# Optimization experiments

Hardware: AMD Instinct MI355X
Metric: run time of the kernel (lower is better)

## Reference

```python
import jax, jax.numpy as jnp
import numpy as np
from math import sqrt

B, L, S, H, E = 4, 2048, 2048, 8, 64
T = 1.0  # softmax temperature


def setup_inputs() -> dict:
    key = jax.random.key(0)
    kq, kk, kv = jax.random.split(key, 3)
    q = jax.random.normal(kq, (B, L, H, E), dtype=jnp.float32)
    k = jax.random.normal(kk, (B, S, H, E), dtype=jnp.float32)
    v = jax.random.normal(kv, (B, S, H, E), dtype=jnp.float32)
    mask = jnp.zeros((B, L), dtype=jnp.bool_)  # unused by the module, kept for signature fidelity
    return {"q": q, "k": k, "v": v, "mask": mask}


def reference(q, k, v, mask):
    Bq, Lq, Hq, Eq = q.shape
    # [B,L,H,E] -> [B,H,E,L]; FFT over time axis
    xq = jnp.transpose(q, (0, 2, 3, 1))
    xk = jnp.transpose(k, (0, 2, 3, 1))
    xv = jnpp_t = jnp.transpose(v, (0, 2, 3, 1))
    xq_ft = jnp.fft.rfft(xq, axis=-1, norm='ortho')   # [B,H,E,Lf]
    xk_ft = jnp.fft.rfft(xk, axis=-1, norm='ortho')   # [B,H,E,Sf]
    xv_ft = jnp.fft.rfft(xv, axis=-1, norm='ortho')   # [B,H,E,Sf]
    # complex frequency-domain scores [B,H,Lf,Sf]
    scores = jnp.einsum('bhex,bhey->bhxy', xq_ft, jnp.conj(xk_ft)) / sqrt(Eq)
    # activation == 'softmax': softmax over |scores|/T, then real-weighted complex mix
    attn = jax.nn.softmax(jnp.abs(scores) / T, axis=-1)
    xqkv_ft = jnp.einsum('bhxy,bhey->bhex', attn.astype(xv_ft.dtype), xv_ft)  # [B,H,E,Lf]
    out = jnp.fft.irfft(xqkv_ft, n=Lq, axis=-1, norm='ortho')  # [B,H,E,L]
    return jnp.transpose(out, (0, 3, 1, 2))  # [B,L,H,E]
```

## Files before the change

kernel.cpp:

```cpp
#include <hip/hip_runtime.h>
#include <hip/hip_bf16.h>
#include <math.h>

#define LOGN  11
#define NN    2048
#define LOGM  10
#define MM    1024
#define NF    1025
#define NYP   1056
#define TWO_PI 6.283185307179586f
#define INV_SQRT_N 0.022097086912079608f
#define INV_SCALE  0.044194173824159216f
#define LOG2E      1.4426950408889634f

#define PAD(i) ((i) + ((i) >> 4))
#define MMP   1088
#define TWP   816

typedef __attribute__((ext_vector_type(8))) short bhalf8;
typedef __attribute__((ext_vector_type(4))) float f32x4;

#define MFMA16(a, b, c) __builtin_amdgcn_mfma_f32_16x16x32_bf16(a, b, c, 0, 0, 0)

#define GLD16(gp, lp)                                                              \
    __builtin_amdgcn_global_load_lds(                                              \
        (const __attribute__((address_space(1))) void*)(gp),                       \
        (__attribute__((address_space(3))) void*)(lp), 16, 0, 0)

#define CVTPK(dst, lo, hi) \
    asm("v_cvt_pk_bf16_f32 %0, %1, %2" : "=v"(dst) : "v"(lo), "v"(hi))

#define EXP2F(dst, src) \
    asm("v_exp_f32 %0, %1" : "=v"(dst) : "v"(src))

__device__ __forceinline__ unsigned short f2bf(float f) {
    union { float f; unsigned u; } v; v.f = f;
    unsigned r = v.u + 0x7FFFu + ((v.u >> 16) & 1u);
    return (unsigned short)(r >> 16);
}
__device__ __forceinline__ float bf2f(unsigned short h) {
    union { unsigned u; float f; } v; v.u = ((unsigned)h) << 16;
    return v.f;
}

__device__ __forceinline__ float2 cmul(float2 x, float2 w) {
    return make_float2(x.x * w.x - x.y * w.y, x.x * w.y + x.y * w.x);
}

template<bool FWD>
__device__ __forceinline__ void r4(float2& a, float2& b, float2& c, float2& d) {
    float2 apc = make_float2(a.x + c.x, a.y + c.y);
    float2 amc = make_float2(a.x - c.x, a.y - c.y);
    float2 bpd = make_float2(b.x + d.x, b.y + d.y);
    float2 bmd = make_float2(b.x - d.x, b.y - d.y);
    a = make_float2(apc.x + bpd.x, apc.y + bpd.y);
    c = make_float2(apc.x - bpd.x, apc.y - bpd.y);
    if (FWD) {
        b = make_float2(amc.x + bmd.y, amc.y - bmd.x);
        d = make_float2(amc.x - bmd.y, amc.y + bmd.x);
    } else {
        b = make_float2(amc.x - bmd.y, amc.y + bmd.x);
        d = make_float2(amc.x + bmd.y, amc.y - bmd.x);
    }
}

template<bool FWD>
__device__ __forceinline__ void s0s1(float2 x[16], const float2* tw) {
    #pragma unroll
    for (int c = 0; c < 4; c++)
        r4<FWD>(x[c], x[4 + c], x[8 + c], x[12 + c]);
    #pragma unroll
    for (int i = 0; i < 4; i++) {
        float2 w1 = tw[PAD(64 * i)], w2 = tw[PAD(128 * i)], w3 = tw[PAD(192 * i)];
        x[4 * i + 1] = cmul(x[4 * i + 1], w1);
        x[4 * i + 2] = cmul(x[4 * i + 2], w2);
        x[4 * i + 3] = cmul(x[4 * i + 3], w3);
        r4<FWD>(x[4 * i], x[4 * i + 1], x[4 * i + 2], x[4 * i + 3]);
    }
}

template<bool FWD>
__device__ __forceinline__ void fft_mid(float2* bufS, const float2* tw, int q, int r)
{
    {
        float2 v[4][4];
        #pragma unroll
        for (int d = 0; d < 4; d++)
            #pragma unroll
            for (int c = 0; c < 4; c++)
                v[d][c] = bufS[PAD(256 * q + 64 * d + 16 * c + r)];
        float2 w1 = tw[PAD(16 * r)], w2 = tw[PAD(32 * r)], w3 = tw[PAD(48 * r)];
        #pragma unroll
        for (int d = 0; d < 4; d++) {
            v[d][1] = cmul(v[d][1], w1);
            v[d][2] = cmul(v[d][2], w2);
            v[d][3] = cmul(v[d][3], w3);
            r4<FWD>(v[d][0], v[d][1], v[d][2], v[d][3]);
        }
        #pragma unroll
        for (int c = 0; c < 4; c++) {
            int e = 4 * (16 * c + r);
            float2 u1 = tw[PAD(e)], u2 = tw[PAD(2 * e)], u3 = tw[PAD(3 * e)];
            v[1][c] = cmul(v[1][c], u1);
            v[2][c] = cmul(v[2][c], u2);
            v[3][c] = cmul(v[3][c], u3);
            r4<FWD>(v[0][c], v[1][c], v[2][c], v[3][c]);
        }
        #pragma unroll
        for (int d = 0; d < 4; d++)
            #pragma unroll
            for (int c = 0; c < 4; c++)
                bufS[PAD(256 * q + 64 * d + 16 * c + r)] = v[d][c];
    }
    __syncthreads();
    {
        #pragma unroll
        for (int k = 0; k < 4; k++) {
            int p4 = 16 * q + r + 64 * k;
            float2 a = bufS[PAD(p4)];
            float2 b = bufS[PAD(p4 + 256)];
            float2 c = bufS[PAD(p4 + 512)];
            float2 d = bufS[PAD(p4 + 768)];
            b = cmul(b, tw[PAD(p4)]);
            c = cmul(c, tw[PAD(2 * p4)]);
            d = cmul(d, tw[PAD(3 * p4)]);
            r4<FWD>(a, b, c, d);
            bufS[PAD(p4)]       = a;
            bufS[PAD(p4 + 256)] = b;
            bufS[PAD(p4 + 512)] = c;
            bufS[PAD(p4 + 768)] = d;
        }
    }
    __syncthreads();
}

__global__ __launch_bounds__(256) void tr_fwd(const float* __restrict__ q,
                                              const float* __restrict__ k,
                                              const float* __restrict__ v,
                                              unsigned short* __restrict__ ttr,
                                              float2* __restrict__ twf,
                                              float2* __restrict__ twi,
                                              float2* __restrict__ rc)
{
    __shared__ float Ts[64][65];
    int tt     = blockIdx.x;
    int h      = blockIdx.y;
    int z      = blockIdx.z;
    int tensor = z >> 2;
    int b      = z & 3;
    int tid    = threadIdx.x;
    int t0     = tt * 64;

    if (z == 0 && h == 0 && tt < 5) {
        int i = tt * 256 + tid;
        if (i < 768) {
            float ang = TWO_PI * (float)i / (float)MM;
            float sv, cv;
            __sincosf(ang, &sv, &cv);
            twf[i] = make_float2(cv, -sv);
            twi[i] = make_float2(cv,  sv);
        }
        if (i < 1025) {
            float ang = TWO_PI * (float)i / (float)NN;
            float sv, cv;
            __sincosf(ang, &sv, &cv);
            rc[i] = make_float2(cv, sv);
        }
    }

    const float* in = (tensor == 0) ? q : (tensor == 1) ? k : v;

    {
        int tl = tid >> 2, ec = (tid & 3) * 16;
        const float* src = in + ((size_t)b * 2048 + t0 + tl) * 512 + h * 64 + ec;
        #pragma unroll
        for (int m = 0; m < 4; m++) {
            float4 v4 = *(const float4*)(src + m * 4);
            Ts[tl][ec + m * 4 + 0] = v4.x;
            Ts[tl][ec + m * 4 + 1] = v4.y;
            Ts[tl][ec + m * 4 + 2] = v4.z;
            Ts[tl][ec + m * 4 + 3] = v4.w;
        }
    }
    __syncthreads();
    {
        int el = tid >> 2, tc = (tid & 3) * 16;
        size_t row = ((size_t)(tensor * 32 + b * 8 + h)) * 64 + el;
        unsigned short* dst = ttr + row * 2048 + t0 + tc;
        #pragma unroll
        for (int m = 0; m < 4; m++) {
            float a0 = Ts[tc + m * 4 + 0][el], a1 = Ts[tc + m * 4 + 1][el];
            float a2 = Ts[tc + m * 4 + 2][el], a3 = Ts[tc + m * 4 + 3][el];
            unsigned u0, u1;
            CVTPK(u0, a0, a1);
            CVTPK(u1, a2, a3);
            uint2 o; o.x = u0; o.y = u1;
            *(uint2*)(dst + m * 4) = o;
        }
    }
}

__global__ __launch_bounds__(128) void fft_fwd(const unsigned short* __restrict__ ttr,
                                               const float2* __restrict__ twg,
                                               const float2* __restrict__ rc,
                                               unsigned short* __restrict__ Pq,
                                               unsigned short* __restrict__ Pk,
                                               unsigned short* __restrict__ Pv)
{
    __shared__ float2 buf[2][MMP];
    __shared__ float2 tw[TWP];

    int g  = blockIdx.x;
    int t  = threadIdx.x;
    int w  = t >> 6, tp = t & 63;
    int q4 = tp >> 4, r = tp & 15;
    int G  = ((tp & 3) << 4) | (tp & 12) | (tp >> 4);

    int s      = 2 * g + w;
    int p      = s % 96;
    int e      = s / 96;
    int tensor = p / 32;
    int bh     = p % 32;

    unsigned short* plane = (tensor == 0) ? Pq : (tensor == 1) ? Pk : Pv;
    float scl = (tensor == 0) ? (INV_SQRT_N * 0.125f * LOG2E) : INV_SQRT_N;
    int vk3 = (tensor == 2) ? (((e >> 2) & 3) << 3) : 0;
    unsigned short* dre  = plane + ((size_t)bh * 128 + e) * NYP;
    unsigned short* dim_ = dre + (size_t)64 * NYP;
    const unsigned short* src = ttr + ((size_t)p * 64 + e) * 2048;

    #pragma unroll
    for (int i = t; i < 768; i += 128) tw[PAD(i)] = twg[i];

    float2* bufS = buf[w];

    float2 x[16];
    #pragma unroll
    for (int k = 0; k < 16; k++) {
        unsigned pr = *(const unsigned*)(src + 2 * (tp + 64 * k));
        x[k] = make_float2(bf2f((unsigned short)(pr & 0xFFFFu)),
                           bf2f((unsigned short)(pr >> 16)));
    }
    s0s1<true>(x, tw);
    #pragma unroll
    for (int k = 0; k < 16; k++)
        bufS[PAD(16 * G + 4 * (k & 3) + (k >> 2))] = x[k];
    __syncthreads();

    fft_mid<true>(bufS, tw, q4, r);

#define RPOINT(Ai, Bi, CX, CY, XR, XI) do {                                \
        float Ex = 0.5f * (Ai.x + Bi.x), Ey = 0.5f * (Ai.y - Bi.y);        \
        float Dx = 0.5f * (Ai.x - Bi.x), Dy = 0.5f * (Ai.y + Bi.y);        \
        float Ox = Dy, Oy = -Dx;                                           \
        XR = (Ex + (CX) * Ox + (CY) * Oy) * scl;                           \
        XI = (Ey + (CX) * Oy - (CY) * Ox) * scl;                           \
    } while (0)

    #pragma unroll
    for (int i = 0; i < 8; i++) {
        int kk = 2 * tp + 128 * i;
        float2 A0 = bufS[PAD(kk)];
        float2 B0 = bufS[PAD((MM - kk) & (MM - 1))];
        float2 A1 = bufS[PAD(kk + 1)];
        float2 B1 = bufS[PAD(MM - kk - 1)];
        float4 rq = *(const float4*)(&rc[kk]);
        float Xr0, Xi0, Xr1, Xi1;
        RPOINT(A0, B0, rq.x, rq.y, Xr0, Xi0);
        RPOINT(A1, B1, rq.z, rq.w, Xr1, Xi1);
        unsigned ur, ui;
        CVTPK(ur, Xr0, Xr1);
        CVTPK(ui, Xi0, Xi1);
        int ks = kk ^ vk3;
        *(unsigned*)(dre + ks)  = ur;
        *(unsigned*)(dim_ + ks) = ui;
    }
    if (tp < 16) {
        unsigned ur = 0, ui = 0;
        if (tp == 0) {
            float2 A = bufS[PAD(0)];
            float Xr = (A.x - A.y) * scl;
            float zz = 0.f;
            CVTPK(ur, Xr, zz);
        }
        int ks = (1024 + 2 * tp) ^ vk3;
        *(unsigned*)(dre + ks)  = ur;
        *(unsigned*)(dim_ + ks) = ui;
    }
#undef RPOINT
}

__global__ __launch_bounds__(256) void qkpack(const unsigned short* __restrict__ Pq,
                                              const unsigned short* __restrict__ Pk,
                                              unsigned short* __restrict__ Qp,
                                              unsigned short* __restrict__ Kp)
{
    __shared__ unsigned short Ts[32][136];
    int y0  = blockIdx.x * 32;
    int bh  = blockIdx.y;
    int tsr = blockIdx.z;
    int tid = threadIdx.x;

    const unsigned short* srcp = (tsr == 0) ? Pq : Pk;
    unsigned short* dstp       = (tsr == 0) ? Qp : Kp;

    {
        int kk = tid >> 1, seg = tid & 1;
        const unsigned short* sp = srcp + ((size_t)bh * 128 + kk) * NYP + y0 + seg * 16;
        uint4 va = *(const uint4*)sp;
        uint4 vb = *(const uint4*)(sp + 8);
        const unsigned short* pa = (const unsigned short*)&va;
        const unsigned short* pb = (const unsigned short*)&vb;
        #pragma unroll
        for (int j = 0; j < 8; j++) Ts[seg * 16 + j][kk] = pa[j];
        #pragma unroll
        for (int j = 0; j < 8; j++) Ts[seg * 16 + 8 + j][kk] = pb[j];
    }
    __syncthreads();
    {
        int y = tid >> 3, c = tid & 7;
        uint4 lo = *(const uint4*)&Ts[y][c * 16];
        uint4 hi = *(const uint4*)&Ts[y][c * 16 + 8];
        char* rowb = (char*)(dstp + ((size_t)bh * NYP + y0 + y) * 128);
        if (tsr == 0) {
            *(uint4*)(rowb + c * 32)      = lo;
            *(uint4*)(rowb + c * 32 + 16) = hi;
        } else {
            int s = y & 7;
            *(uint4*)(rowb + (((2 * c)     ^ s) << 4)) = lo;
            *(uint4*)(rowb + (((2 * c + 1) ^ s) << 4)) = hi;
        }
    }
}

struct FlashShared {
    union {
        struct {
            unsigned short Ks[2][32][128];
            unsigned short Vs[2][128][32];
        } kv;
        unsigned short OutT[128][136];
    } u;
    unsigned short Ps[8][16][40];
};

template<int NH>
__global__ __launch_bounds__(512) void flash_mfma(
    const unsigned short* __restrict__ Qp,
    const unsigned short* __restrict__ Kp,
    const unsigned short* __restrict__ Vt,
    unsigned short* __restrict__ nb0,
    unsigned short* __restrict__ nb1,
    float* __restrict__ lbuf)
{
    __shared__ FlashShared S;

    int g    = blockIdx.x;
    int bh   = g & 31;
    int idx  = g >> 5;
    int half = idx / 9;
    int x0   = (idx % 9) * 128;
    int tid  = threadIdx.x;
    int w    = tid >> 6;
    int lane = tid & 63;
    int qd   = lane >> 4;
    int col  = lane & 15;

    int xrow = x0 + w * 16 + col;
    int xq   = min(xrow, 1024);
    const unsigned short* qb = Qp + ((size_t)bh * NYP + xq) * 128 + qd * 8;
    bhalf8 Are[4], Aim[4];
    #pragma unroll
    for (int ks = 0; ks < 4; ks++) Are[ks] = *(const bhalf8*)(qb + ks * 32);
    Aim[0] = Are[2];
    Aim[1] = Are[3];
    #pragma unroll
    for (int ks = 0; ks < 2; ks++) {
        bhalf8 t = Are[ks];
        unsigned* u = (unsigned*)&t;
        #pragma unroll
        for (int j = 0; j < 4; j++) u[j] ^= 0x80008000u;
        Aim[ks + 2] = t;
    }

    f32x4 O[8];
    #pragma unroll
    for (int n = 0; n < 8; n++) O[n] = (f32x4){0.f, 0.f, 0.f, 0.f};
    float Lacc[4] = {0.f, 0.f, 0.f, 0.f};

    int yt0 = (half * 33) / NH, yt1 = ((half + 1) * 33) / NH;

    const char* ksrc = (const char*)Kp
        + ((size_t)bh * NYP + (size_t)yt0 * 32 + w * 4) * 256 + lane * 16;
    const char* vbase = (const char*)Vt + (size_t)bh * 128 * (NYP * 2);
    const char* vsrc = vbase + ((size_t)(w * 16) + (lane >> 2)) * (NYP * 2)
                       + (size_t)yt0 * 64 + (lane & 3) * 16;

    int sw = col & 7;
    int kco[4];
    #pragma unroll
    for (int ks = 0; ks < 4; ks++) kco[ks] = ((ks * 4 + qd) ^ sw) * 8;
    int vq = (qd ^ ((col >> 2) & 3)) * 8;

    {
        int pb = yt0 & 1;
        GLD16(ksrc, &S.u.kv.Ks[pb][w * 4][0]);
        GLD16(vsrc, &S.u.kv.Vs[pb][w * 16][0]);
        ksrc += 8192; vsrc += 64;
    }

    for (int yt = yt0; yt < yt1; yt++) {
        int cb = yt & 1, nb = cb ^ 1;
        if (yt + 1 < yt1) {
            GLD16(ksrc, &S.u.kv.Ks[nb][w * 4][0]);
            GLD16(vsrc, &S.u.kv.Vs[nb][w * 16][0]);
            ksrc += 8192; vsrc += 64;
            __builtin_amdgcn_sched_barrier(0);
            asm volatile("s_waitcnt vmcnt(2)" ::: "memory");
        } else {
            __builtin_amdgcn_sched_barrier(0);
            asm volatile("s_waitcnt vmcnt(0)" ::: "memory");
        }
        __builtin_amdgcn_sched_barrier(0);
        __builtin_amdgcn_s_barrier();
        __builtin_amdgcn_sched_barrier(0);

        const unsigned short* k0 = &S.u.kv.Ks[cb][col][0];
        const unsigned short* k1 = &S.u.kv.Ks[cb][col + 16][0];

        f32x4 sre[2], sim[2];
        #pragma unroll
        for (int sc = 0; sc < 2; sc++) {
            sre[sc] = (f32x4){0.f, 0.f, 0.f, 0.f};
            sim[sc] = (f32x4){0.f, 0.f, 0.f, 0.f};
        }
        __builtin_amdgcn_s_setprio(1);
        #pragma unroll
        for (int ks = 0; ks < 4; ks++) {
            bhalf8 b0 = *(const bhalf8*)(k0 + kco[ks]);
            bhalf8 b1 = *(const bhalf8*)(k1 + kco[ks]);
            sre[0] = MFMA16(Are[ks], b0, sre[0]);
            sim[0] = MFMA16(Aim[ks], b0, sim[0]);
            sre[1] = MFMA16(Are[ks], b1, sre[1]);
            sim[1] = MFMA16(Aim[ks], b1, sim[1]);
        }
        __builtin_amdgcn_s_setprio(0);

        #pragma unroll
        for (int r = 0; r < 4; r++) {
            float re0 = sre[0][r], im0 = sim[0][r];
            float re1 = sre[1][r], im1 = sim[1][r];
            float s0 = __builtin_amdgcn_sqrtf(fmaf(re0, re0, im0 * im0));
            float s1 = __builtin_amdgcn_sqrtf(fmaf(re1, re1, im1 * im1));
            float p0, p1;
            EXP2F(p0, s0);
            EXP2F(p1, s1);
            Lacc[r] += p0 + p1;
            unsigned up;
            CVTPK(up, p0, p1);
            S.Ps[w][qd * 4 + r][col]      = (unsigned short)up;
            S.Ps[w][qd * 4 + r][col + 16] = (unsigned short)(up >> 16);
        }

        bhalf8 pa = *(const bhalf8*)&S.Ps[w][col][qd * 8];
        __builtin_amdgcn_s_setprio(1);
        #pragma unroll
        for (int n = 0; n < 8; n++) {
            bhalf8 bv = *(const bhalf8*)&S.u.kv.Vs[cb][n * 16 + col][vq];
            O[n] = MFMA16(pa, bv, O[n]);
        }
        __builtin_amdgcn_s_setprio(0);

        asm volatile("s_waitcnt lgkmcnt(0)" ::: "memory");
        __builtin_amdgcn_sched_barrier(0);
        __builtin_amdgcn_s_barrier();
        __builtin_amdgcn_sched_barrier(0);
    }

    #pragma unroll
    for (int r = 0; r < 4; r++) {
        float ls = Lacc[r];
        ls += __shfl_xor(ls, 1);
        ls += __shfl_xor(ls, 2);
        ls += __shfl_xor(ls, 4);
        ls += __shfl_xor(ls, 8);
        if (yt1 == 33) ls -= 31.0f;
        int x = x0 + w * 16 + qd * 4 + r;
        if (x <= 1024 && col == 0)
            lbuf[((size_t)half * 32 + bh) * NYP + x] = ls;
    }

    const size_t HSZ = (size_t)32 * 128 * NYP;
    unsigned short* nplane = (half < 2 ? nb0 : nb1) + (size_t)(half & 1) * HSZ;

    __syncthreads();
    #pragma unroll
    for (int n = 0; n < 8; n++) {
        unsigned u0, u1;
        CVTPK(u0, O[n][0], O[n][1]);
        CVTPK(u1, O[n][2], O[n][3]);
        *(unsigned*)&S.u.OutT[n * 16 + col][w * 16 + qd * 4]     = u0;
        *(unsigned*)&S.u.OutT[n * 16 + col][w * 16 + qd * 4 + 2] = u1;
    }
    __syncthreads();
    {
        int kk2 = tid >> 2, seg = tid & 3;
        int xg  = x0 + seg * 32;
        if (xg < NYP) {
            unsigned short* dst = nplane + ((size_t)bh * 128 + kk2) * NYP + xg;
            const unsigned short* srcl = &S.u.OutT[kk2][seg * 32];
            #pragma unroll
            for (int m = 0; m < 4; m++)
                *(uint4*)(dst + m * 8) = *(const uint4*)(srcl + m * 8);
        }
    }
}

template<int NH>
__global__ __launch_bounds__(128) void fft_inv(const unsigned short* __restrict__ nb0,
                                               const unsigned short* __restrict__ nb1,
                                               const float2* __restrict__ twg,
                                               const float2* __restrict__ rc,
                                               const float* __restrict__ lbuf,
                                               float* __restrict__ st)
{
    __shared__ float2 buf[2][MMP];
    __shared__ float2 tw[TWP];

    int g  = blockIdx.x;
    int t  = threadIdx.x;
    int w  = t >> 6, tp = t & 63;
    int q4 = tp >> 4, r = tp & 15;
    int G  = ((tp & 3) << 4) | (tp & 12) | (tp >> 4);

    int sidx = 2 * g + w;
    int e    = sidx & 63;
    int bh   = sidx >> 6;

    #pragma unroll
    for (int i = t; i < 768; i += 128) tw[PAD(i)] = twg[i];

    const size_t HSZ = (size_t)32 * 128 * NYP;
    const unsigned short* pre[NH];
    const unsigned short* pim[NH];
    const float* lb[NH];
    #pragma unroll
    for (int h = 0; h < NH; h++) {
        const unsigned short* base = (h < 2 ? nb0 : nb1) + (size_t)(h & 1) * HSZ;
        pre[h] = base + ((size_t)bh * 128 + e) * NYP;
        pim[h] = base + ((size_t)bh * 128 + 64 + e) * NYP;
        lb[h]  = lbuf + ((size_t)h * 32 + bh) * NYP;
    }

    float2* bufS = buf[w];

    float2 x[16];
    #pragma unroll
    for (int k = 0; k < 16; k++) {
        int kk = tp + 64 * k;
        int x1 = kk, x2 = 1024 - kk;
        float d1 = 0.f, d2 = 0.f;
        float Axs = 0.f, Ays = 0.f, Bxs = 0.f, Bys = 0.f;
        #pragma unroll
        for (int h = 0; h < NH; h++) {
            d1 += lb[h][x1];
            d2 += lb[h][x2];
            Axs += bf2f(pre[h][x1]);
            Ays += bf2f(pim[h][x1]);
            Bxs += bf2f(pre[h][x2]);
            Bys += bf2f(pim[h][x2]);
        }
        float iv1 = 1.f / d1, iv2 = 1.f / d2;
        float Ax = Axs * iv1, Ay = Ays * iv1;
        float Bx = Bxs * iv2, By = -(Bys * iv2);
        float Ex = 0.5f * (Ax + Bx), Ey = 0.5f * (Ay + By);
        float Dx = 0.5f * (Ax - Bx), Dy = 0.5f * (Ay - By);
        float2 rcv = rc[kk];
        float Ox = Dx * rcv.x - Dy * rcv.y;
        float Oy = Dx * rcv.y + Dy * rcv.x;
        x[k] = make_float2(Ex - Oy, Ey + Ox);
    }
    s0s1<false>(x, tw);
    #pragma unroll
    for (int k = 0; k < 16; k++)
        bufS[PAD(16 * G + 4 * (k & 3) + (k >> 2))] = x[k];
    __syncthreads();

    fft_mid<false>(bufS, tw, q4, r);

    float* dst = st + ((size_t)bh * 64 + e) * 2048;
    #pragma unroll
    for (int i = 0; i < 16; i++) {
        int j = tp + 64 * i;
        float2 z = bufS[PAD(j)];
        *(float2*)&dst[2 * j] = make_float2(z.x * INV_SCALE, z.y * INV_SCALE);
    }
}

__global__ __launch_bounds__(256) void out_tr(const float* __restrict__ st,
                                              float* __restrict__ out)
{
    __shared__ float Ts[64][65];
    int tt  = blockIdx.x;
    int h   = blockIdx.y;
    int b   = blockIdx.z;
    int tid = threadIdx.x;
    int bh  = b * 8 + h;

    {
        int e = tid >> 2, tc = (tid & 3) * 16;
        const float* src = st + ((size_t)bh * 64 + e) * 2048 + tt * 64 + tc;
        #pragma unroll
        for (int m = 0; m < 4; m++) {
            float4 v4 = *(const float4*)(src + m * 4);
            Ts[e][tc + m * 4 + 0] = v4.x;
            Ts[e][tc + m * 4 + 1] = v4.y;
            Ts[e][tc + m * 4 + 2] = v4.z;
            Ts[e][tc + m * 4 + 3] = v4.w;
        }
    }
    __syncthreads();
    {
        int t = tid >> 2, ec = (tid & 3) * 16;
        float* dst = out + (size_t)b * 2048 * 512 + (size_t)(tt * 64 + t) * 512
                     + h * 64 + ec;
        #pragma unroll
        for (int m = 0; m < 4; m++) {
            float4 v4;
            v4.x = Ts[ec + m * 4 + 0][t];
            v4.y = Ts[ec + m * 4 + 1][t];
            v4.z = Ts[ec + m * 4 + 2][t];
            v4.w = Ts[ec + m * 4 + 3][t];
            *(float4*)(dst + m * 4) = v4;
        }
    }
}

extern "C" void kernel_launch(void* const* d_in, const int* in_sizes, int n_in,
                              void* d_out, int out_size, void* d_ws, size_t ws_size,
                              hipStream_t stream)
{
    const float* q = (const float*)d_in[0];
    const float* k = (const float*)d_in[1];
    const float* v = (const float*)d_in[2];
    float* out = (float*)d_out;

    char* ws = (char*)d_ws;
    const size_t PL = (size_t)32 * 128 * NYP * sizeof(unsigned short);
    unsigned short* Pq = (unsigned short*)(ws);
    unsigned short* Pk = (unsigned short*)(ws + PL);
    unsigned short* Pv = (unsigned short*)(ws + 2 * PL);
    unsigned short* ttr = (unsigned short*)(ws + 3 * PL);
    unsigned short* Qp = (unsigned short*)(ws + 3 * PL);
    unsigned short* Kp = (unsigned short*)(ws + 4 * PL);
    float* st = (float*)(ws + 3 * PL);

    const size_t lbuf4 = (size_t)4 * 32 * NYP * sizeof(float);
    const size_t lbuf2 = (size_t)2 * 32 * NYP * sizeof(float);
    const size_t TBL   = (size_t)(768 + 768 + 1025) * sizeof(float2);
    bool big = ws_size >= 7 * PL + lbuf4 + TBL;

    char* tb = big ? (ws + 7 * PL + lbuf4) : (ws + 5 * PL + lbuf2);
    float2* twf = (float2*)tb;
    float2* twi = twf + 768;
    float2* rc  = twi + 768;

    hipLaunchKernelGGL(tr_fwd, dim3(32, 8, 12), dim3(256), 0, stream,
                       q, k, v, ttr, twf, twi, rc);
    hipLaunchKernelGGL(fft_fwd, dim3(3 * 1024), dim3(128), 0, stream,
                       ttr, twf, rc, Pq, Pk, Pv);
    hipLaunchKernelGGL(qkpack, dim3(33, 32, 2), dim3(256), 0, stream,
                       Pq, Pk, Qp, Kp);

    if (big) {
        unsigned short* nb0 = (unsigned short*)(ws);
        unsigned short* nb1 = (unsigned short*)(ws + 5 * PL);
        float* lbuf = (float*)(ws + 7 * PL);
        hipLaunchKernelGGL((flash_mfma<4>), dim3(9 * 4 * 32), dim3(512), 0, stream,
                           Qp, Kp, Pv, nb0, nb1, lbuf);
        hipLaunchKernelGGL((fft_inv<4>), dim3(1024), dim3(128), 0, stream,
                           nb0, nb1, twi, rc, lbuf, st);
    } else {
        unsigned short* nb0 = (unsigned short*)(ws);
        float* lbuf = (float*)(ws + 5 * PL);
        hipLaunchKernelGGL((flash_mfma<2>), dim3(9 * 2 * 32), dim3(512), 0, stream,
                           Qp, Kp, Pv, nb0, nb0, lbuf);
        hipLaunchKernelGGL((fft_inv<2>), dim3(1024), dim3(128), 0, stream,
                           nb0, nb0, twi, rc, lbuf, st);
    }

    hipLaunchKernelGGL(out_tr, dim3(32, 8, 4), dim3(256), 0, stream,
                       st, out);
}
```

Measured before the change: 202.5 us.

## Fuse Q/K transpose-pack into flash kernel, dropping qkpack launch

Removes the separate qkpack kernel that transposed the frequency-domain Q and K into row-major swizzled layouts. The flash kernel now reads Q with strided scalar gathers and loads K tiles into registers, then scatters them into swizzled shared memory itself, overlapping this with the MFMA work. Workspace buffers are reassigned so nb0 and st no longer alias the removed Qp/Kp regions. This saves one launch and a full global round-trip of Q and K, at the cost of uncoalesced Q loads and extra LDS scatter stores inside the main loop.

```diff
diff --git a/kernel.cpp b/kernel.cpp
--- a/kernel.cpp
+++ b/kernel.cpp
@@ -290,49 +290,6 @@
 #undef RPOINT
 }
 
-__global__ __launch_bounds__(256) void qkpack(const unsigned short* __restrict__ Pq,
-                                              const unsigned short* __restrict__ Pk,
-                                              unsigned short* __restrict__ Qp,
-                                              unsigned short* __restrict__ Kp)
-{
-    __shared__ unsigned short Ts[32][136];
-    int y0  = blockIdx.x * 32;
-    int bh  = blockIdx.y;
-    int tsr = blockIdx.z;
-    int tid = threadIdx.x;
-
-    const unsigned short* srcp = (tsr == 0) ? Pq : Pk;
-    unsigned short* dstp       = (tsr == 0) ? Qp : Kp;
-
-    {
-        int kk = tid >> 1, seg = tid & 1;
-        const unsigned short* sp = srcp + ((size_t)bh * 128 + kk) * NYP + y0 + seg * 16;
-        uint4 va = *(const uint4*)sp;
-        uint4 vb = *(const uint4*)(sp + 8);
-        const unsigned short* pa = (const unsigned short*)&va;
-        const unsigned short* pb = (const unsigned short*)&vb;
-        #pragma unroll
-        for (int j = 0; j < 8; j++) Ts[seg * 16 + j][kk] = pa[j];
-        #pragma unroll
-        for (int j = 0; j < 8; j++) Ts[seg * 16 + 8 + j][kk] = pb[j];
-    }
-    __syncthreads();
-    {
-        int y = tid >> 3, c = tid & 7;
-        uint4 lo = *(const uint4*)&Ts[y][c * 16];
-        uint4 hi = *(const uint4*)&Ts[y][c * 16 + 8];
-        char* rowb = (char*)(dstp + ((size_t)bh * NYP + y0 + y) * 128);
-        if (tsr == 0) {
-            *(uint4*)(rowb + c * 32)      = lo;
-            *(uint4*)(rowb + c * 32 + 16) = hi;
-        } else {
-            int s = y & 7;
-            *(uint4*)(rowb + (((2 * c)     ^ s) << 4)) = lo;
-            *(uint4*)(rowb + (((2 * c + 1) ^ s) << 4)) = hi;
-        }
-    }
-}
-
 struct FlashShared {
     union {
         struct {
@@ -346,8 +303,8 @@
 
 template<int NH>
 __global__ __launch_bounds__(512) void flash_mfma(
-    const unsigned short* __restrict__ Qp,
-    const unsigned short* __restrict__ Kp,
+    const unsigned short* __restrict__ Pq,
+    const unsigned short* __restrict__ Pk,
     const unsigned short* __restrict__ Vt,
     unsigned short* __restrict__ nb0,
     unsigned short* __restrict__ nb1,
@@ -368,10 +325,16 @@
 
     int xrow = x0 + w * 16 + col;
     int xq   = min(xrow, 1024);
-    const unsigned short* qb = Qp + ((size_t)bh * NYP + xq) * 128 + qd * 8;
+    const unsigned short* qbase = Pq + (size_t)bh * 128 * NYP + xq;
     bhalf8 Are[4], Aim[4];
     #pragma unroll
-    for (int ks = 0; ks < 4; ks++) Are[ks] = *(const bhalf8*)(qb + ks * 32);
+    for (int ks = 0; ks < 4; ks++) {
+        bhalf8 a;
+        #pragma unroll
+        for (int j = 0; j < 8; j++)
+            a[j] = (short)qbase[(size_t)(ks * 32 + qd * 8 + j) * NYP];
+        Are[ks] = a;
+    }
     Aim[0] = Are[2];
     Aim[1] = Are[3];
     #pragma unroll
@@ -390,8 +353,12 @@
 
     int yt0 = (half * 33) / NH, yt1 = ((half + 1) * 33) / NH;
 
-    const char* ksrc = (const char*)Kp
-        + ((size_t)bh * NYP + (size_t)yt0 * 32 + w * 4) * 256 + lane * 16;
+    const unsigned short* kb = Pk + ((size_t)bh * 128 + w * 16 + (lane >> 2)) * NYP
+                               + (size_t)yt0 * 32 + (lane & 3) * 8;
+    int ck3 = w * 2 + (lane >> 5);
+    int ck7 = (lane >> 2) & 7;
+    int rb  = (lane & 3) * 8;
+
     const char* vbase = (const char*)Vt + (size_t)bh * 128 * (NYP * 2);
     const char* vsrc = vbase + ((size_t)(w * 16) + (lane >> 2)) * (NYP * 2)
                        + (size_t)yt0 * 64 + (lane & 3) * 16;
@@ -402,19 +369,28 @@
     for (int ks = 0; ks < 4; ks++) kco[ks] = ((ks * 4 + qd) ^ sw) * 8;
     int vq = (qd ^ ((col >> 2) & 3)) * 8;
 
+    uint4 kreg;
     {
         int pb = yt0 & 1;
-        GLD16(ksrc, &S.u.kv.Ks[pb][w * 4][0]);
-        GLD16(vsrc, &S.u.kv.Vs[pb][w * 16][0]);
-        ksrc += 8192; vsrc += 64;
+        kreg = *(const uint4*)kb;  kb += 32;
+        GLD16(vsrc, &S.u.kv.Vs[pb][w * 16][0]);  vsrc += 64;
+        __builtin_amdgcn_sched_barrier(0);
+        asm volatile("s_waitcnt vmcnt(0)" ::: "memory");
+        __builtin_amdgcn_sched_barrier(0);
+        const unsigned short* kv = (const unsigned short*)&kreg;
+        #pragma unroll
+        for (int j = 0; j < 8; j++)
+            S.u.kv.Ks[pb][rb + j][((ck3 ^ j) << 3) | ck7] = kv[j];
+        asm volatile("s_waitcnt lgkmcnt(0)" ::: "memory");
+        __builtin_amdgcn_sched_barrier(0);
     }
 
     for (int yt = yt0; yt < yt1; yt++) {
         int cb = yt & 1, nb = cb ^ 1;
-        if (yt + 1 < yt1) {
-            GLD16(ksrc, &S.u.kv.Ks[nb][w * 4][0]);
-            GLD16(vsrc, &S.u.kv.Vs[nb][w * 16][0]);
-            ksrc += 8192; vsrc += 64;
+        bool has_next = (yt + 1 < yt1);
+        if (has_next) {
+            kreg = *(const uint4*)kb;  kb += 32;
+            GLD16(vsrc, &S.u.kv.Vs[nb][w * 16][0]);  vsrc += 64;
             __builtin_amdgcn_sched_barrier(0);
             asm volatile("s_waitcnt vmcnt(2)" ::: "memory");
         } else {
@@ -471,6 +447,15 @@
         }
         __builtin_amdgcn_s_setprio(0);
 
+        if (has_next) {
+            __builtin_amdgcn_sched_barrier(0);
+            asm volatile("s_waitcnt vmcnt(1)" ::: "memory");
+            __builtin_amdgcn_sched_barrier(0);
+            const unsigned short* kv = (const unsigned short*)&kreg;
+            #pragma unroll
+            for (int j = 0; j < 8; j++)
+                S.u.kv.Ks[nb][rb + j][((ck3 ^ j) << 3) | ck7] = kv[j];
+        }
         asm volatile("s_waitcnt lgkmcnt(0)" ::: "memory");
         __builtin_amdgcn_sched_barrier(0);
         __builtin_amdgcn_s_barrier();
@@ -651,9 +636,7 @@
     unsigned short* Pk = (unsigned short*)(ws + PL);
     unsigned short* Pv = (unsigned short*)(ws + 2 * PL);
     unsigned short* ttr = (unsigned short*)(ws + 3 * PL);
-    unsigned short* Qp = (unsigned short*)(ws + 3 * PL);
-    unsigned short* Kp = (unsigned short*)(ws + 4 * PL);
-    float* st = (float*)(ws + 3 * PL);
+    float* st = (float*)(ws);
 
     const size_t lbuf4 = (size_t)4 * 32 * NYP * sizeof(float);
     const size_t lbuf2 = (size_t)2 * 32 * NYP * sizeof(float);
@@ -669,22 +652,20 @@
                        q, k, v, ttr, twf, twi, rc);
     hipLaunchKernelGGL(fft_fwd, dim3(3 * 1024), dim3(128), 0, stream,
                        ttr, twf, rc, Pq, Pk, Pv);
-    hipLaunchKernelGGL(qkpack, dim3(33, 32, 2), dim3(256), 0, stream,
-                       Pq, Pk, Qp, Kp);
 
     if (big) {
-        unsigned short* nb0 = (unsigned short*)(ws);
+        unsigned short* nb0 = (unsigned short*)(ws + 3 * PL);
         unsigned short* nb1 = (unsigned short*)(ws + 5 * PL);
         float* lbuf = (float*)(ws + 7 * PL);
         hipLaunchKernelGGL((flash_mfma<4>), dim3(9 * 4 * 32), dim3(512), 0, stream,
-                           Qp, Kp, Pv, nb0, nb1, lbuf);
+                           Pq, Pk, Pv, nb0, nb1, lbuf);
         hipLaunchKernelGGL((fft_inv<4>), dim3(1024), dim3(128), 0, stream,
                            nb0, nb1, twi, rc, lbuf, st);
     } else {
-        unsigned short* nb0 = (unsigned short*)(ws);
+        unsigned short* nb0 = (unsigned short*)(ws + 3 * PL);
         float* lbuf = (float*)(ws + 5 * PL);
         hipLaunchKernelGGL((flash_mfma<2>), dim3(9 * 2 * 32), dim3(512), 0, stream,
-                           Qp, Kp, Pv, nb0, nb0, lbuf);
+                           Pq, Pk, Pv, nb0, nb0, lbuf);
         hipLaunchKernelGGL((fft_inv<2>), dim3(1024), dim3(128), 0, stream,
                            nb0, nb0, twi, rc, lbuf, st);
     }
```

Result: no change. 204.2 us (+0.8%).
